# Kernel optimization log

Measured on AMD Instinct MI355X. Metric: run time of the kernel, lower is better.

The kernel has to match this reference:

```python
import jax, jax.numpy as jnp
import numpy as np

N = 50000
E = 800000


def sage_conv(x, edge_index, W_l, b_l, W_r):
    """PyG SAGEConv with mean aggregation.

    out = lin_l(mean_{j in N(i)} x_j) + lin_r(x_i)
    lin_l has bias, lin_r (root weight) has no bias.
    """
    src, dst = edge_index[0], edge_index[1]
    n = x.shape[0]
    msg_sum = jax.ops.segment_sum(x[src], dst, num_segments=n)          # [N, F]
    cnt = jax.ops.segment_sum(jnp.ones((edge_index.shape[1],), x.dtype), dst,
                              num_segments=n)                           # [N]
    mean = msg_sum / jnp.maximum(cnt, 1.0)[:, None]
    return mean @ W_l + b_l + x @ W_r


def setup_inputs() -> dict:
    key = jax.random.key(0)
    ks = jax.random.split(key, 10)
    dims = [(128, 128), (128, 128), (128, 64)]
    inp = {
        "x": jax.random.normal(ks[0], (N, 128), dtype=jnp.float32),
        "edge_index": jax.random.randint(ks[1], (2, E), 0, N, dtype=jnp.int64),
    }
    for i, (fi, fo) in enumerate(dims):
        scale = 1.0 / np.sqrt(fi)
        inp[f"W_l{i}"] = jax.random.uniform(ks[2 + 3 * i - (3 * i) % 1], (fi, fo), jnp.float32, -scale, scale)
        inp[f"b_l{i}"] = jnp.zeros((fo,), jnp.float32)
        inp[f"W_r{i}"] = jax.random.uniform(jax.random.fold_in(ks[3], i), (fi, fo), jnp.float32, -scale, scale)
        inp[f"W_l{i}"] = jax.random.uniform(jax.random.fold_in(ks[2], i), (fi, fo), jnp.float32, -scale, scale)
    return inp


def reference(x, edge_index, W_l0, b_l0, W_r0, W_l1, b_l1, W_r1, W_l2, b_l2, W_r2):
    # Layer 1 + relu (dropout identity in eval mode)
    h = jax.nn.relu(sage_conv(x, edge_index, W_l0, b_l0, W_r0))
    # Layer 2 + relu
    h = jax.nn.relu(sage_conv(h, edge_index, W_l1, b_l1, W_r1))
    # Output layer (no activation)
    return sage_conv(h, edge_index, W_l2, b_l2, W_r2)
```

## Files before the change

### kernel.cpp

```cpp
#include <hip/hip_runtime.h>

static inline int ceil_div(int a, int b) { return (a + b - 1) / b; }

typedef __attribute__((ext_vector_type(8))) short short8;
typedef __attribute__((ext_vector_type(4))) float f32x4;

__device__ __forceinline__ ushort bf16_rne(float v) {
  uint u = __float_as_uint(v);
  return (ushort)((u + 0x7FFFu + ((u >> 16) & 1u)) >> 16);
}


__global__ void k_zero_int(int* __restrict__ p, int n) {
  int i = blockIdx.x * blockDim.x + threadIdx.x;
  if (i < n) p[i] = 0;
}

__global__ void k_cvt(const float* __restrict__ in, ushort* __restrict__ outp, int n8) {
  int i = blockIdx.x * blockDim.x + threadIdx.x;
  if (i >= n8) return;
  const float4* ip = (const float4*)(in + (size_t)i * 8);
  float4 a = ip[0], b = ip[1];
  uint p0 = (uint)bf16_rne(a.x) | ((uint)bf16_rne(a.y) << 16);
  uint p1 = (uint)bf16_rne(a.z) | ((uint)bf16_rne(a.w) << 16);
  uint p2 = (uint)bf16_rne(b.x) | ((uint)bf16_rne(b.y) << 16);
  uint p3 = (uint)bf16_rne(b.z) | ((uint)bf16_rne(b.w) << 16);
  ((uint4*)outp)[i] = make_uint4(p0, p1, p2, p3);
}


__global__ void k_count_rank(const int* __restrict__ dst, int* __restrict__ cnt,
                             ushort* __restrict__ rank, int e) {
  int i0 = (blockIdx.x * blockDim.x + threadIdx.x) * 4;
  if (i0 >= e) return;
  int d[4], r[4];
  if (i0 + 3 < e) {
    int4 dv = *(const int4*)(dst + i0);
    d[0] = dv.x; d[1] = dv.y; d[2] = dv.z; d[3] = dv.w;
  } else {
#pragma unroll
    for (int j = 0; j < 4; ++j) d[j] = (i0 + j < e) ? dst[i0 + j] : 0;
  }
#pragma unroll
  for (int j = 0; j < 4; ++j)
    if (i0 + j < e) r[j] = atomicAdd(&cnt[d[j]], 1);
  if (i0 + 3 < e) {
    ushort4 rv;
    rv.x = (ushort)r[0]; rv.y = (ushort)r[1];
    rv.z = (ushort)r[2]; rv.w = (ushort)r[3];
    *(ushort4*)(rank + i0) = rv;
  } else {
#pragma unroll
    for (int j = 0; j < 4; ++j)
      if (i0 + j < e) rank[i0 + j] = (ushort)r[j];
  }
}

#define SCAN_BS 256
#define SCAN_VPT 4
#define SCAN_CHUNK (SCAN_BS * SCAN_VPT)

__global__ __launch_bounds__(SCAN_BS) void k_blocksum(const int* __restrict__ cnt,
                                                      int* __restrict__ partial, int n) {
  __shared__ int s[SCAN_BS / 64];
  const int tid = threadIdx.x;
  const int base = blockIdx.x * SCAN_CHUNK;
  int sum = 0;
#pragma unroll
  for (int j = 0; j < SCAN_VPT; ++j) {
    int i = base + tid + j * SCAN_BS;
    if (i < n) sum += cnt[i];
  }
#pragma unroll
  for (int off = 32; off > 0; off >>= 1) sum += __shfl_down(sum, off, 64);
  if ((tid & 63) == 0) s[tid >> 6] = sum;
  __syncthreads();
  if (tid == 0) {
    int t = 0;
#pragma unroll
    for (int w = 0; w < SCAN_BS / 64; ++w) t += s[w];
    partial[blockIdx.x] = t;
  }
}

__global__ __launch_bounds__(256) void k_scan_partials(int* __restrict__ partial, int p,
                                                       int* __restrict__ row_ptr, int n_nodes) {
  __shared__ int s[256];
  const int tid = threadIdx.x;
  int carry = 0;
  for (int base = 0; base < p; base += 256) {
    int i = base + tid;
    int v = (i < p) ? partial[i] : 0;
    s[tid] = v;
    __syncthreads();
    for (int off = 1; off < 256; off <<= 1) {
      int t = (tid >= off) ? s[tid - off] : 0;
      __syncthreads();
      s[tid] += t;
      __syncthreads();
    }
    if (i < p) partial[i] = carry + s[tid] - v;
    int tot = s[255];
    __syncthreads();
    carry += tot;
  }
  if (tid == 0) row_ptr[n_nodes] = carry;
}

__global__ __launch_bounds__(SCAN_BS) void k_scatter(const int* __restrict__ cnt,
                                                     const int* __restrict__ partial,
                                                     int* __restrict__ row_ptr,
                                                     float* __restrict__ inv, int n) {
  __shared__ int s[SCAN_BS];
  const int tid = threadIdx.x;
  const int base = blockIdx.x * SCAN_CHUNK;
  const int i0 = base + tid * SCAN_VPT;
  int v[SCAN_VPT];
  int cv[SCAN_VPT];
  int sum = 0;
#pragma unroll
  for (int j = 0; j < SCAN_VPT; ++j) {
    int i = i0 + j;
    int c = (i < n) ? cnt[i] : 0;
    cv[j] = c;
    v[j] = sum;
    sum += c;
  }
  s[tid] = sum;
  __syncthreads();
  for (int off = 1; off < SCAN_BS; off <<= 1) {
    int t = (tid >= off) ? s[tid - off] : 0;
    __syncthreads();
    s[tid] += t;
    __syncthreads();
  }
  const int excl = partial[blockIdx.x] + s[tid] - sum;
#pragma unroll
  for (int j = 0; j < SCAN_VPT; ++j) {
    int i = i0 + j;
    if (i < n) {
      row_ptr[i] = excl + v[j];
      inv[i] = 1.0f / (float)(cv[j] > 1 ? cv[j] : 1);
    }
  }
}

__global__ void k_place(const int* __restrict__ src, const int* __restrict__ dst,
                        const ushort* __restrict__ rank, const int* __restrict__ row_ptr,
                        ushort* __restrict__ csr16, int e) {
  int i0 = (blockIdx.x * blockDim.x + threadIdx.x) * 4;
  if (i0 >= e) return;
  if (i0 + 3 < e) {
    int4 dv = *(const int4*)(dst + i0);
    int4 sv = *(const int4*)(src + i0);
    ushort4 rv = *(const ushort4*)(rank + i0);
    int p0 = row_ptr[dv.x], p1 = row_ptr[dv.y], p2 = row_ptr[dv.z], p3 = row_ptr[dv.w];
    csr16[p0 + rv.x] = (ushort)sv.x;
    csr16[p1 + rv.y] = (ushort)sv.y;
    csr16[p2 + rv.z] = (ushort)sv.z;
    csr16[p3 + rv.w] = (ushort)sv.w;
  } else {
#pragma unroll
    for (int j = 0; j < 4; ++j) {
      int i = i0 + j;
      if (i < e) csr16[row_ptr[dst[i]] + rank[i]] = (ushort)src[i];
    }
  }
}

template <int FOUT>
__global__ void k_pack(const float* __restrict__ Wl, const float* __restrict__ Wr,
                       ushort* __restrict__ hi) {
  constexpr int NCOL = 2 * FOUT;
  constexpr int NCHUNK = 4 * NCOL * 4;
  int ct = blockIdx.x * 256 + threadIdx.x;
  if (ct >= NCHUNK) return;
  const int g = ct & 3;
  const int nn = (ct >> 2) % NCOL;
  const int kt = ct / (4 * NCOL);
  uint hw[4];
#pragma unroll
  for (int w = 0; w < 4; ++w) {
    uint h2[2];
#pragma unroll
    for (int t = 0; t < 2; ++t) {
      int j = 2 * w + t;
      int k = kt * 32 + g * 8 + j;
      float v = (nn < FOUT) ? Wl[k * FOUT + nn] : Wr[k * FOUT + (nn - FOUT)];
      h2[t] = (uint)bf16_rne(v);
    }
    hw[w] = h2[0] | (h2[1] << 16);
  }
  ((uint4*)hi)[ct] = make_uint4(hw[0], hw[1], hw[2], hw[3]);
}

template <int FOUT>
__global__ __launch_bounds__(256) void k_gemm2b(const ushort* __restrict__ Hb,
                                                const ushort* __restrict__ Whi,
                                                const float* __restrict__ bias,
                                                ushort* __restrict__ Zb,
                                                ushort* __restrict__ Rb, int n) {
  constexpr int NCOL = 2 * FOUT;
  constexpr int NT = NCOL / 64;
  constexpr int MT = 2;
  __shared__ uint4 sA[32 * 16];

  const int tid = threadIdx.x;
  const int lane = tid & 63;
  const int wave = tid >> 6;
  const int row0 = blockIdx.x * 32;

  const int n0 = wave * (NCOL / 4);
  const int g16 = lane >> 4;
  const int l16 = lane & 15;

#pragma unroll
  for (int c = tid; c < 512; c += 256) {
    int srow = c >> 4, col16 = c & 15;
    int g = row0 + srow;
    uint4 v = make_uint4(0u, 0u, 0u, 0u);
    if (g < n) v = *(const uint4*)(Hb + (size_t)g * 128 + col16 * 8);
    sA[srow * 16 + (col16 ^ (srow & 7))] = v;
  }

  short8 bh[NT], bhN[NT];
#pragma unroll
  for (int nt = 0; nt < NT; ++nt) {
    size_t chunk = (size_t)(0 * NCOL + n0 + nt * 16 + l16) * 4 + g16;
    bh[nt] = *(const short8*)(Whi + chunk * 8);
  }
  __syncthreads();

  f32x4 acc[MT][NT];
#pragma unroll
  for (int mt = 0; mt < MT; ++mt)
#pragma unroll
    for (int nt = 0; nt < NT; ++nt) acc[mt][nt] = (f32x4)(0.f);

#pragma unroll
  for (int kt = 0; kt < 4; ++kt) {
    short8 a[MT];
#pragma unroll
    for (int mt = 0; mt < MT; ++mt) {
      int row = mt * 16 + l16;
      int slot = (kt * 4 + g16) ^ (row & 7);
      a[mt] = *(const short8*)&sA[row * 16 + slot];
    }
    if (kt < 3) {
#pragma unroll
      for (int nt = 0; nt < NT; ++nt) {
        size_t chunk = (size_t)((kt + 1) * NCOL + n0 + nt * 16 + l16) * 4 + g16;
        bhN[nt] = *(const short8*)(Whi + chunk * 8);
      }
    }
#pragma unroll
    for (int mt = 0; mt < MT; ++mt)
#pragma unroll
      for (int nt = 0; nt < NT; ++nt)
        acc[mt][nt] = __builtin_amdgcn_mfma_f32_16x16x32_bf16(a[mt], bh[nt], acc[mt][nt], 0, 0, 0);
    if (kt < 3) {
#pragma unroll
      for (int nt = 0; nt < NT; ++nt) bh[nt] = bhN[nt];
    }
  }

#pragma unroll
  for (int nt = 0; nt < NT; ++nt) {
    int col = n0 + nt * 16 + l16;
    bool isR = col >= FOUT;
    int cw = isR ? col - FOUT : col;
    float badd = isR ? bias[cw] : 0.f;
    ushort* base = isR ? Rb : Zb;
#pragma unroll
    for (int mt = 0; mt < MT; ++mt) {
#pragma unroll
      for (int j = 0; j < 4; ++j) {
        int row = row0 + mt * 16 + g16 * 4 + j;
        if (row < n) base[(size_t)row * FOUT + cw] = bf16_rne(acc[mt][nt][j] + badd);
      }
    }
  }
}

template <int FOUT, bool RELU, bool OUTB>
__global__ __launch_bounds__(256) void k_agg2(const ushort* __restrict__ Zb,
                                              const ushort* __restrict__ Rb,
                                              const int* __restrict__ row_ptr,
                                              const ushort* __restrict__ csr16,
                                              const float* __restrict__ inv,
                                              void* __restrict__ outp, int n) {
  constexpr int FL = FOUT / 8;
  constexpr int EG = 64 / FL;
  const int lane = threadIdx.x & 63;
  const int node = blockIdx.x * 4 + (threadIdx.x >> 6);
  if (node >= n) return;
  const int c = lane % FL;
  const int eg = lane / FL;

  const int e0 = row_ptr[node];
  const int m = row_ptr[node + 1] - e0;
  const uint4* Z4 = (const uint4*)Zb;

  float acc[8];
#pragma unroll
  for (int k = 0; k < 8; ++k) acc[k] = 0.f;

  int t = eg;
  while (t < m) {
    int ss[4];
#pragma unroll
    for (int j = 0; j < 4; ++j) {
      int tj = t + j * EG;
      int tc = (tj < m) ? tj : (m - 1);
      ss[j] = csr16[e0 + tc];
    }
    uint4 z[4];
#pragma unroll
    for (int j = 0; j < 4; ++j) z[j] = Z4[(size_t)ss[j] * FL + c];
#pragma unroll
    for (int j = 0; j < 4; ++j) {
      if (t + j * EG < m) {
        const uint* zw = (const uint*)&z[j];
#pragma unroll
        for (int w = 0; w < 4; ++w) {
          acc[2 * w]     += __uint_as_float(zw[w] << 16);
          acc[2 * w + 1] += __uint_as_float(zw[w] & 0xFFFF0000u);
        }
      }
    }
    t += 4 * EG;
  }

#pragma unroll
  for (int off = FL; off < 64; off <<= 1) {
#pragma unroll
    for (int k = 0; k < 8; ++k) acc[k] += __shfl_xor(acc[k], off, 64);
  }

  if (eg == 0) {
    const float iv = inv[node];
    uint4 rw = ((const uint4*)Rb)[(size_t)node * FL + c];
    const uint* rp = (const uint*)&rw;
    float o[8];
#pragma unroll
    for (int w = 0; w < 4; ++w) {
      o[2 * w]     = fmaf(acc[2 * w],     iv, __uint_as_float(rp[w] << 16));
      o[2 * w + 1] = fmaf(acc[2 * w + 1], iv, __uint_as_float(rp[w] & 0xFFFF0000u));
    }
    if (RELU) {
#pragma unroll
      for (int k = 0; k < 8; ++k) o[k] = fmaxf(o[k], 0.f);
    }
    if (OUTB) {
      uint p[4];
#pragma unroll
      for (int w = 0; w < 4; ++w)
        p[w] = (uint)bf16_rne(o[2 * w]) | ((uint)bf16_rne(o[2 * w + 1]) << 16);
      ((uint4*)outp)[(size_t)node * FL + c] = make_uint4(p[0], p[1], p[2], p[3]);
    } else {
      float4* op = (float4*)((float*)outp + (size_t)node * FOUT + c * 8);
      op[0] = make_float4(o[0], o[1], o[2], o[3]);
      op[1] = make_float4(o[4], o[5], o[6], o[7]);
    }
  }
}


extern "C" void kernel_launch(void* const* d_in, const int* in_sizes, int n_in,
                              void* d_out, int out_size, void* d_ws, size_t ws_size,
                              hipStream_t stream) {
  const float* x   = (const float*)d_in[0];
  const int*   ei  = (const int*)d_in[1];
  const float* Wl0 = (const float*)d_in[2];
  const float* bl0 = (const float*)d_in[3];
  const float* Wr0 = (const float*)d_in[4];
  const float* Wl1 = (const float*)d_in[5];
  const float* bl1 = (const float*)d_in[6];
  const float* Wr1 = (const float*)d_in[7];
  const float* Wl2 = (const float*)d_in[8];
  const float* bl2 = (const float*)d_in[9];
  const float* Wr2 = (const float*)d_in[10];
  float* out = (float*)d_out;

  const int N = in_sizes[0] / 128;
  const int E = in_sizes[1] / 2;
  const int* src = ei;
  const int* dst = ei + E;

  char* w = (char*)d_ws;
  auto alloc = [&](size_t bytes) {
    char* p = w;
    w += (bytes + 255) & ~(size_t)255;
    return p;
  };
  int*    cnt     = (int*)alloc((size_t)N * 4);
  int*    row_ptr = (int*)alloc((size_t)(N + 1) * 4);
  ushort* rank    = (ushort*)alloc((size_t)E * 2 + 256);
  ushort* csr16   = (ushort*)alloc((size_t)E * 2 + 256);
  float*  inv     = (float*)alloc((size_t)N * 4);
  int*    partial = (int*)alloc((size_t)ceil_div(N, SCAN_CHUNK) * 4 + 256);
  ushort* Whi0    = (ushort*)alloc((size_t)4 * 256 * 4 * 16);
  ushort* Whi1    = (ushort*)alloc((size_t)4 * 256 * 4 * 16);
  ushort* Whi2    = (ushort*)alloc((size_t)4 * 128 * 4 * 16);
  ushort* XB      = (ushort*)alloc((size_t)N * 128 * 2);
  ushort* BZ      = (ushort*)alloc((size_t)N * 128 * 2);
  ushort* BRb     = (ushort*)alloc((size_t)N * 128 * 2);
  ushort* B0      = (ushort*)alloc((size_t)N * 128 * 2);
  (void)ws_size; (void)n_in; (void)out_size;

  const int P = ceil_div(N, SCAN_CHUNK);

  k_pack<128><<<16, 256, 0, stream>>>(Wl0, Wr0, Whi0);
  k_pack<128><<<16, 256, 0, stream>>>(Wl1, Wr1, Whi1);
  k_pack<64><<<8, 256, 0, stream>>>(Wl2, Wr2, Whi2);
  k_cvt<<<ceil_div(N * 16, 256), 256, 0, stream>>>(x, XB, N * 16);

  k_zero_int<<<ceil_div(N, 256), 256, 0, stream>>>(cnt, N);
  k_count_rank<<<ceil_div(E, 1024), 256, 0, stream>>>(dst, cnt, rank, E);
  k_blocksum<<<P, SCAN_BS, 0, stream>>>(cnt, partial, N);
  k_scan_partials<<<1, 256, 0, stream>>>(partial, P, row_ptr, N);
  k_scatter<<<P, SCAN_BS, 0, stream>>>(cnt, partial, row_ptr, inv, N);
  k_place<<<ceil_div(E, 1024), 256, 0, stream>>>(src, dst, rank, row_ptr, csr16, E);

  k_gemm2b<128><<<ceil_div(N, 32), 256, 0, stream>>>(XB, Whi0, bl0, BZ, BRb, N);
  k_agg2<128, true, true><<<ceil_div(N, 4), 256, 0, stream>>>(BZ, BRb, row_ptr, csr16, inv, B0, N);

  k_gemm2b<128><<<ceil_div(N, 32), 256, 0, stream>>>(B0, Whi1, bl1, BZ, BRb, N);
  k_agg2<128, true, true><<<ceil_div(N, 4), 256, 0, stream>>>(BZ, BRb, row_ptr, csr16, inv, B0, N);

  k_gemm2b<64><<<ceil_div(N, 32), 256, 0, stream>>>(B0, Whi2, bl2, BZ, BRb, N);
  k_agg2<64, false, false><<<ceil_div(N, 4), 256, 0, stream>>>(BZ, BRb, row_ptr, csr16, inv, out, N);
}
```

Baseline: 220.8 us.

## Fuse prep kernels, single-pass lookback scan, deeper gather pipelining in aggregation

Merges the weight-pack, x conversion and count zeroing into one multi-role prep kernel, and replaces the three-kernel scan with a single kernel that uses a decoupled lookback over per-block flags. This removes several launches and their serialization gaps from a short pipeline. The aggregation kernel also issues 8 gathers in flight instead of 4 for the 128-wide layers to hide more memory latency. The lookback spins on flags from earlier blocks, which assumes those blocks are resident or already finished. The flag array holds only 32 entries, so the scan relies on N needing no more than 32 blocks.

Measured after the change: 213.2 us. 3.4% less time.

```diff
diff --git a/kernel.cpp b/kernel.cpp
--- a/kernel.cpp
+++ b/kernel.cpp
@@ -10,22 +10,67 @@
   return (ushort)((u + 0x7FFFu + ((u >> 16) & 1u)) >> 16);
 }
 
-
-__global__ void k_zero_int(int* __restrict__ p, int n) {
-  int i = blockIdx.x * blockDim.x + threadIdx.x;
-  if (i < n) p[i] = 0;
-}
-
-__global__ void k_cvt(const float* __restrict__ in, ushort* __restrict__ outp, int n8) {
-  int i = blockIdx.x * blockDim.x + threadIdx.x;
-  if (i >= n8) return;
-  const float4* ip = (const float4*)(in + (size_t)i * 8);
-  float4 a = ip[0], b = ip[1];
-  uint p0 = (uint)bf16_rne(a.x) | ((uint)bf16_rne(a.y) << 16);
-  uint p1 = (uint)bf16_rne(a.z) | ((uint)bf16_rne(a.w) << 16);
-  uint p2 = (uint)bf16_rne(b.x) | ((uint)bf16_rne(b.y) << 16);
-  uint p3 = (uint)bf16_rne(b.z) | ((uint)bf16_rne(b.w) << 16);
-  ((uint4*)outp)[i] = make_uint4(p0, p1, p2, p3);
+__device__ __forceinline__ void pack_dev(const float* __restrict__ Wl,
+                                         const float* __restrict__ Wr,
+                                         ushort* __restrict__ hi, int ct, int FOUT) {
+  const int NCOL = 2 * FOUT;
+  const int g = ct & 3;
+  const int nn = (ct >> 2) % NCOL;
+  const int kt = ct / (4 * NCOL);
+  uint hw[4];
+#pragma unroll
+  for (int w = 0; w < 4; ++w) {
+    uint h2[2];
+#pragma unroll
+    for (int t = 0; t < 2; ++t) {
+      int j = 2 * w + t;
+      int k = kt * 32 + g * 8 + j;
+      float v = (nn < FOUT) ? Wl[k * FOUT + nn] : Wr[k * FOUT + (nn - FOUT)];
+      h2[t] = (uint)bf16_rne(v);
+    }
+    hw[w] = h2[0] | (h2[1] << 16);
+  }
+  ((uint4*)hi)[ct] = make_uint4(hw[0], hw[1], hw[2], hw[3]);
+}
+
+__global__ void k_prep(const float* __restrict__ Wl0, const float* __restrict__ Wr0,
+                       ushort* __restrict__ hi0,
+                       const float* __restrict__ Wl1, const float* __restrict__ Wr1,
+                       ushort* __restrict__ hi1,
+                       const float* __restrict__ Wl2, const float* __restrict__ Wr2,
+                       ushort* __restrict__ hi2,
+                       const float* __restrict__ x, ushort* __restrict__ xb,
+                       int* __restrict__ cnt, int* __restrict__ bflag,
+                       int n, int zb) {
+  const int b = blockIdx.x;
+  const int tid = threadIdx.x;
+  if (b < 16) {
+    pack_dev(Wl0, Wr0, hi0, b * 256 + tid, 128);
+  } else if (b < 32) {
+    pack_dev(Wl1, Wr1, hi1, (b - 16) * 256 + tid, 128);
+  } else if (b < 40) {
+    pack_dev(Wl2, Wr2, hi2, (b - 32) * 256 + tid, 64);
+  } else if (b < 40 + zb) {
+    int b2 = b - 40;
+    int i0 = b2 * 2048 + tid;
+#pragma unroll
+    for (int j = 0; j < 8; ++j) {
+      int i = i0 + j * 256;
+      if (i < n) cnt[i] = 0;
+    }
+    if (b2 == 0 && tid < 32) bflag[tid] = 0;
+  } else {
+    int i = (b - 40 - zb) * 256 + tid;
+    if (i < n * 16) {
+      const float4* ip = (const float4*)(x + (size_t)i * 8);
+      float4 a = ip[0], bb = ip[1];
+      uint p0 = (uint)bf16_rne(a.x) | ((uint)bf16_rne(a.y) << 16);
+      uint p1 = (uint)bf16_rne(a.z) | ((uint)bf16_rne(a.w) << 16);
+      uint p2 = (uint)bf16_rne(bb.x) | ((uint)bf16_rne(bb.y) << 16);
+      uint p3 = (uint)bf16_rne(bb.z) | ((uint)bf16_rne(bb.w) << 16);
+      ((uint4*)xb)[i] = make_uint4(p0, p1, p2, p3);
+    }
+  }
 }
 
 
@@ -57,66 +102,20 @@
 }
 
 #define SCAN_BS 256
-#define SCAN_VPT 4
+#define SCAN_VPT 8
 #define SCAN_CHUNK (SCAN_BS * SCAN_VPT)
 
-__global__ __launch_bounds__(SCAN_BS) void k_blocksum(const int* __restrict__ cnt,
-                                                      int* __restrict__ partial, int n) {
-  __shared__ int s[SCAN_BS / 64];
+__global__ __launch_bounds__(SCAN_BS) void k_scan_lb(const int* __restrict__ cnt,
+                                                     int* __restrict__ row_ptr,
+                                                     float* __restrict__ inv,
+                                                     int* __restrict__ bflag,
+                                                     int n, int nblocks) {
+  __shared__ int s[SCAN_BS];
+  __shared__ int s_prev;
   const int tid = threadIdx.x;
-  const int base = blockIdx.x * SCAN_CHUNK;
-  int sum = 0;
-#pragma unroll
-  for (int j = 0; j < SCAN_VPT; ++j) {
-    int i = base + tid + j * SCAN_BS;
-    if (i < n) sum += cnt[i];
-  }
-#pragma unroll
-  for (int off = 32; off > 0; off >>= 1) sum += __shfl_down(sum, off, 64);
-  if ((tid & 63) == 0) s[tid >> 6] = sum;
-  __syncthreads();
-  if (tid == 0) {
-    int t = 0;
-#pragma unroll
-    for (int w = 0; w < SCAN_BS / 64; ++w) t += s[w];
-    partial[blockIdx.x] = t;
-  }
-}
-
-__global__ __launch_bounds__(256) void k_scan_partials(int* __restrict__ partial, int p,
-                                                       int* __restrict__ row_ptr, int n_nodes) {
-  __shared__ int s[256];
-  const int tid = threadIdx.x;
-  int carry = 0;
-  for (int base = 0; base < p; base += 256) {
-    int i = base + tid;
-    int v = (i < p) ? partial[i] : 0;
-    s[tid] = v;
-    __syncthreads();
-    for (int off = 1; off < 256; off <<= 1) {
-      int t = (tid >= off) ? s[tid - off] : 0;
-      __syncthreads();
-      s[tid] += t;
-      __syncthreads();
-    }
-    if (i < p) partial[i] = carry + s[tid] - v;
-    int tot = s[255];
-    __syncthreads();
-    carry += tot;
-  }
-  if (tid == 0) row_ptr[n_nodes] = carry;
-}
-
-__global__ __launch_bounds__(SCAN_BS) void k_scatter(const int* __restrict__ cnt,
-                                                     const int* __restrict__ partial,
-                                                     int* __restrict__ row_ptr,
-                                                     float* __restrict__ inv, int n) {
-  __shared__ int s[SCAN_BS];
-  const int tid = threadIdx.x;
-  const int base = blockIdx.x * SCAN_CHUNK;
-  const int i0 = base + tid * SCAN_VPT;
-  int v[SCAN_VPT];
-  int cv[SCAN_VPT];
+  const int bid = blockIdx.x;
+  const int i0 = bid * SCAN_CHUNK + tid * SCAN_VPT;
+  int v[SCAN_VPT], cv[SCAN_VPT];
   int sum = 0;
 #pragma unroll
   for (int j = 0; j < SCAN_VPT; ++j) {
@@ -134,7 +133,20 @@
     s[tid] += t;
     __syncthreads();
   }
-  const int excl = partial[blockIdx.x] + s[tid] - sum;
+  const int btotal = s[SCAN_BS - 1];
+  if (tid == 0) {
+    atomicExch(&bflag[bid], btotal + 1);
+    int prev = 0;
+    for (int b = 0; b < bid; ++b) {
+      int f;
+      do { f = atomicAdd(&bflag[b], 0); } while (f == 0);
+      prev += f - 1;
+    }
+    s_prev = prev;
+    if (bid == nblocks - 1) row_ptr[n] = prev + btotal;
+  }
+  __syncthreads();
+  const int excl = s_prev + s[tid] - sum;
 #pragma unroll
   for (int j = 0; j < SCAN_VPT; ++j) {
     int i = i0 + j;
@@ -169,32 +181,6 @@
 }
 
 template <int FOUT>
-__global__ void k_pack(const float* __restrict__ Wl, const float* __restrict__ Wr,
-                       ushort* __restrict__ hi) {
-  constexpr int NCOL = 2 * FOUT;
-  constexpr int NCHUNK = 4 * NCOL * 4;
-  int ct = blockIdx.x * 256 + threadIdx.x;
-  if (ct >= NCHUNK) return;
-  const int g = ct & 3;
-  const int nn = (ct >> 2) % NCOL;
-  const int kt = ct / (4 * NCOL);
-  uint hw[4];
-#pragma unroll
-  for (int w = 0; w < 4; ++w) {
-    uint h2[2];
-#pragma unroll
-    for (int t = 0; t < 2; ++t) {
-      int j = 2 * w + t;
-      int k = kt * 32 + g * 8 + j;
-      float v = (nn < FOUT) ? Wl[k * FOUT + nn] : Wr[k * FOUT + (nn - FOUT)];
-      h2[t] = (uint)bf16_rne(v);
-    }
-    hw[w] = h2[0] | (h2[1] << 16);
-  }
-  ((uint4*)hi)[ct] = make_uint4(hw[0], hw[1], hw[2], hw[3]);
-}
-
-template <int FOUT>
 __global__ __launch_bounds__(256) void k_gemm2b(const ushort* __restrict__ Hb,
                                                 const ushort* __restrict__ Whi,
                                                 const float* __restrict__ bias,
@@ -291,6 +277,7 @@
                                               void* __restrict__ outp, int n) {
   constexpr int FL = FOUT / 8;
   constexpr int EG = 64 / FL;
+  constexpr int DEPTH = (FL == 16) ? 8 : 4;
   const int lane = threadIdx.x & 63;
   const int node = blockIdx.x * 4 + (threadIdx.x >> 6);
   if (node >= n) return;
@@ -307,18 +294,18 @@
 
   int t = eg;
   while (t < m) {
-    int ss[4];
-#pragma unroll
-    for (int j = 0; j < 4; ++j) {
+    int ss[DEPTH];
+#pragma unroll
+    for (int j = 0; j < DEPTH; ++j) {
       int tj = t + j * EG;
       int tc = (tj < m) ? tj : (m - 1);
       ss[j] = csr16[e0 + tc];
     }
-    uint4 z[4];
-#pragma unroll
-    for (int j = 0; j < 4; ++j) z[j] = Z4[(size_t)ss[j] * FL + c];
-#pragma unroll
-    for (int j = 0; j < 4; ++j) {
+    uint4 z[DEPTH];
+#pragma unroll
+    for (int j = 0; j < DEPTH; ++j) z[j] = Z4[(size_t)ss[j] * FL + c];
+#pragma unroll
+    for (int j = 0; j < DEPTH; ++j) {
       if (t + j * EG < m) {
         const uint* zw = (const uint*)&z[j];
 #pragma unroll
@@ -328,7 +315,7 @@
         }
       }
     }
-    t += 4 * EG;
+    t += DEPTH * EG;
   }
 
 #pragma unroll
@@ -395,10 +382,10 @@
   };
   int*    cnt     = (int*)alloc((size_t)N * 4);
   int*    row_ptr = (int*)alloc((size_t)(N + 1) * 4);
+  int*    bflag   = (int*)alloc(32 * 4);
   ushort* rank    = (ushort*)alloc((size_t)E * 2 + 256);
   ushort* csr16   = (ushort*)alloc((size_t)E * 2 + 256);
   float*  inv     = (float*)alloc((size_t)N * 4);
-  int*    partial = (int*)alloc((size_t)ceil_div(N, SCAN_CHUNK) * 4 + 256);
   ushort* Whi0    = (ushort*)alloc((size_t)4 * 256 * 4 * 16);
   ushort* Whi1    = (ushort*)alloc((size_t)4 * 256 * 4 * 16);
   ushort* Whi2    = (ushort*)alloc((size_t)4 * 128 * 4 * 16);
@@ -408,18 +395,15 @@
   ushort* B0      = (ushort*)alloc((size_t)N * 128 * 2);
   (void)ws_size; (void)n_in; (void)out_size;
 
-  const int P = ceil_div(N, SCAN_CHUNK);
-
-  k_pack<128><<<16, 256, 0, stream>>>(Wl0, Wr0, Whi0);
-  k_pack<128><<<16, 256, 0, stream>>>(Wl1, Wr1, Whi1);
-  k_pack<64><<<8, 256, 0, stream>>>(Wl2, Wr2, Whi2);
-  k_cvt<<<ceil_div(N * 16, 256), 256, 0, stream>>>(x, XB, N * 16);
-
-  k_zero_int<<<ceil_div(N, 256), 256, 0, stream>>>(cnt, N);
+  const int ZB = ceil_div(N, 2048);
+  const int PS = ceil_div(N, SCAN_CHUNK);
+  const int PREP_B = 40 + ZB + ceil_div(N * 16, 256);
+
+  k_prep<<<PREP_B, 256, 0, stream>>>(Wl0, Wr0, Whi0, Wl1, Wr1, Whi1,
+                                     Wl2, Wr2, Whi2, x, XB, cnt, bflag, N, ZB);
+
   k_count_rank<<<ceil_div(E, 1024), 256, 0, stream>>>(dst, cnt, rank, E);
-  k_blocksum<<<P, SCAN_BS, 0, stream>>>(cnt, partial, N);
-  k_scan_partials<<<1, 256, 0, stream>>>(partial, P, row_ptr, N);
-  k_scatter<<<P, SCAN_BS, 0, stream>>>(cnt, partial, row_ptr, inv, N);
+  k_scan_lb<<<PS, SCAN_BS, 0, stream>>>(cnt, row_ptr, inv, bflag, N, PS);
   k_place<<<ceil_div(E, 1024), 256, 0, stream>>>(src, dst, rank, row_ptr, csr16, E);
 
   k_gemm2b<128><<<ceil_div(N, 32), 256, 0, stream>>>(XB, Whi0, bl0, BZ, BRb, N);
```
